# Performance work log

Hardware: AMD Instinct MI355X
Metric: run time of the kernel (lower is better)

The kernel has to match this reference:

```python
import jax, jax.numpy as jnp
import numpy as np

EPS = 1e-5  # InstanceNorm2d default eps (affine=False, biased var)

def setup_inputs() -> dict:
    key = jax.random.key(0)
    ks = jax.random.split(key, 16)
    B, N, KV, H = 16, 196, 960, 4
    chs = [64, 128, 256, 512]
    inp = {}
    inp['emb0'] = jax.random.normal(ks[0], (B, N, chs[0]), jnp.float32)
    inp['emb1'] = jax.random.normal(ks[1], (B, N, chs[1]), jnp.float32)
    inp['emb2'] = jax.random.normal(ks[2], (B, N, chs[2]), jnp.float32)
    inp['emb3'] = jax.random.normal(ks[3], (B, N, chs[3]), jnp.float32)
    inp['emb_all'] = jax.random.normal(ks[4], (B, N, KV), jnp.float32)
    for i, ch in enumerate(chs):
        inp[f'Wq{i}'] = jax.random.normal(ks[5 + i], (H, ch, ch), jnp.float32) * (1.0 / np.sqrt(ch))
        inp[f'Wo{i}'] = jax.random.normal(ks[9 + i], (ch, ch), jnp.float32) * (1.0 / np.sqrt(ch))
    inp['Wk'] = jax.random.normal(ks[13], (H, KV, KV), jnp.float32) * (1.0 / np.sqrt(KV))
    inp['Wv'] = jax.random.normal(ks[14], (H, KV, KV), jnp.float32) * (1.0 / np.sqrt(KV))
    return inp

def _attend(emb, Wq, Wo, K, V, inv_sqrt_kv):
    # Q: per-head Linear(ch,ch) then transpose(-1,-2) -> [B,H,ch,N]
    Q = jnp.einsum('bnc,hdc->bhdn', emb, Wq)
    # scores: [B,H,ch,KV]
    scores = jnp.einsum('bhdn,bhnj->bhdj', Q, K) * inv_sqrt_kv
    # InstanceNorm2d over the (ch, KV) plane per (batch, head), no affine
    m = scores.mean(axis=(-2, -1), keepdims=True)
    v = scores.var(axis=(-2, -1), keepdims=True)
    probs = jax.nn.softmax((scores - m) * jax.lax.rsqrt(v + EPS), axis=-1)
    # ctx = (probs @ V^T).permute(0,3,2,1).mean(dim=3) -> mean over heads: [B,N,ch]
    ctx = jnp.einsum('bhdj,bhnj->bnd', probs, V) / probs.shape[1]
    # out projection: nn.Linear(ch,ch) -> x @ Wo^T
    return jnp.einsum('bnd,ed->bne', ctx, Wo)

def reference(emb0, emb1, emb2, emb3, emb_all, Wq0, Wq1, Wq2, Wq3, Wk, Wv, Wo0, Wo1, Wo2, Wo3):
    KV = emb_all.shape[-1]
    inv_sqrt_kv = jnp.float32(1.0 / np.sqrt(KV))
    # multi-head K/V: stacked per-head Linear(KV,KV) -> [B,H,N,KV]
    K = jnp.einsum('bnk,hjk->bhnj', emb_all, Wk)
    V = jnp.einsum('bnk,hjk->bhnj', emb_all, Wv)
    o0 = _attend(emb0, Wq0, Wo0, K, V, inv_sqrt_kv)
    o1 = _attend(emb1, Wq1, Wo1, K, V, inv_sqrt_kv)
    o2 = _attend(emb2, Wq2, Wo2, K, V, inv_sqrt_kv)
    o3 = _attend(emb3, Wq3, Wo3, K, V, inv_sqrt_kv)
    return (o0, o1, o2, o3)
```

## Files before the change

kernel.cpp:

```cpp
#include <hip/hip_runtime.h>

typedef _Float16 half_t;
typedef _Float16 h8 __attribute__((ext_vector_type(8)));
typedef _Float16 h4 __attribute__((ext_vector_type(4)));
typedef float f4v __attribute__((ext_vector_type(4)));

__device__ __forceinline__ void async16(half_t* l, const half_t* g)
{
    __builtin_amdgcn_global_load_lds(
        (const __attribute__((address_space(1))) void*)g,
        (__attribute__((address_space(3))) void*)l,
        16, 0, 0);
}

struct PrepArgs {
    const float* src[15];
    half_t* dst[15];
    int n[15];
    int mode[15];
    int lg2[15];
};

__global__ __launch_bounds__(256) void prep_k(PrepArgs a)
{
    const int seg = blockIdx.y;
    const int i8 = (blockIdx.x * 256 + threadIdx.x) * 8;
    if (i8 >= a.n[seg]) return;
    const float* s = a.src[seg] + i8;
    f4v v0 = *(const f4v*)s;
    f4v v1 = *(const f4v*)(s + 4);
    h8 o;
    o[0] = (half_t)v0[0]; o[1] = (half_t)v0[1]; o[2] = (half_t)v0[2]; o[3] = (half_t)v0[3];
    o[4] = (half_t)v1[0]; o[5] = (half_t)v1[1]; o[6] = (half_t)v1[2]; o[7] = (half_t)v1[3];
    if (a.mode[seg] == 0) {
        *(h8*)(a.dst[seg] + i8) = o;
    } else {
        const int lg = a.lg2[seg], ch = 1 << lg;
        const int e = i8 >> lg, d = i8 & (ch - 1);
        half_t* base = a.dst[seg] + ((long long)e << (lg + 2)) + d;
        #pragma unroll
        for (int r = 0; r < 4; ++r) *(h8*)(base + r * ch) = o;
    }
}

__device__ __forceinline__ h8 ldtile(const half_t* __restrict__ base, int row, int kb,
                                     int ld, int rowLim, int Klim)
{
    h8 v = {0, 0, 0, 0, 0, 0, 0, 0};
    if (row >= rowLim) return v;
    const half_t* p = base + (long long)row * ld + kb;
    if (kb + 8 <= Klim) return *(const h8*)p;
    #pragma unroll
    for (int e = 0; e < 8; ++e) if (kb + e < Klim) v[e] = p[e];
    return v;
}

struct BP {
    const half_t* A[6]; const half_t* B[6]; void* C[6];
    int Mlim[6], Nlim[6], Klim[6], nKt[6], lda[6], ldb[6], ldc[6];
    int divA[6]; long long sAhi[6], sAlo[6];
    int divB[6]; long long sBhi[6], sBlo[6];
    int divC[6]; long long sChi[6], sClo[6];
    int outMode[6];
    float alpha[6];
    int mT[6], nT[6];
    int cumEnd[5];
    int totW;
};

__global__ __launch_bounds__(128)
void gemm_b(BP P)
{
    __shared__ __align__(16) half_t SM[64 * 72];
    half_t (*As)[32] = (half_t(*)[32])SM;
    half_t (*Bs)[32] = (half_t(*)[32])(SM + 2048);

    int b = blockIdx.x;
    int s = 0, basev = 0;
    #pragma unroll
    for (int i = 0; i < 5; ++i) if (b >= P.cumEnd[i]) { s = i + 1; basev = P.cumEnd[i]; }
    b -= basev;
    const int mTl = P.mT[s], nTl = P.nT[s];
    const int mt = b % mTl;
    const int t2 = b / mTl;
    const int nt = t2 % nTl;
    const int z  = t2 / nTl;

    const half_t* A  = P.A[s] + (long long)(z / P.divA[s]) * P.sAhi[s] + (long long)(z % P.divA[s]) * P.sAlo[s];
    const half_t* Bp = P.B[s] + (long long)(z / P.divB[s]) * P.sBhi[s] + (long long)(z % P.divB[s]) * P.sBlo[s];
    const int Mlim = P.Mlim[s], Klim = P.Klim[s], nKt = P.nKt[s];
    const int lda = P.lda[s], ldb = P.ldb[s], ldc = P.ldc[s];
    const float alpha = P.alpha[s];
    const int m0 = mt * 64, n0 = nt * 64;
    const int tid = threadIdx.x;
    const int lane = tid & 63, w = tid >> 6;
    const int l15 = lane & 15, q = lane >> 4;

    const int r0 = tid >> 2, kg = tid & 3;
    const int r1 = r0 + 32;

    f4v acc[4][2];
    #pragma unroll
    for (int i = 0; i < 4; ++i)
        #pragma unroll
        for (int j = 0; j < 2; ++j) acc[i][j] = (f4v){0.f, 0.f, 0.f, 0.f};

    for (int kt = 0; kt < nKt; ++kt) {
        const int kb = kt * 32 + kg * 8;
        h8 a0 = ldtile(A, m0 + r0, kb, lda, Mlim, Klim);
        h8 a1 = ldtile(A, m0 + r1, kb, lda, Mlim, Klim);
        h8 b0 = ldtile(Bp, n0 + r0, kb, ldb, 1 << 30, Klim);
        h8 b1 = ldtile(Bp, n0 + r1, kb, ldb, 1 << 30, Klim);
        __syncthreads();
        *(h8*)&As[r0][kg * 8] = a0;
        *(h8*)&As[r1][kg * 8] = a1;
        *(h8*)&Bs[r0][kg * 8] = b0;
        *(h8*)&Bs[r1][kg * 8] = b1;
        __syncthreads();
        h8 af[4], bf[2];
        #pragma unroll
        for (int mti = 0; mti < 4; ++mti) af[mti] = *(h8*)&As[mti * 16 + l15][q * 8];
        #pragma unroll
        for (int nti = 0; nti < 2; ++nti) bf[nti] = *(h8*)&Bs[w * 32 + nti * 16 + l15][q * 8];
        #pragma unroll
        for (int mti = 0; mti < 4; ++mti)
            #pragma unroll
            for (int nti = 0; nti < 2; ++nti)
                acc[mti][nti] = __builtin_amdgcn_mfma_f32_16x16x32_f16(af[mti], bf[nti], acc[mti][nti], 0, 0, 0);
    }

    float* Cz = (float*)P.C[s] + (long long)(z / P.divC[s]) * P.sChi[s] + (long long)(z % P.divC[s]) * P.sClo[s];
    #pragma unroll
    for (int mti = 0; mti < 4; ++mti)
        #pragma unroll
        for (int r = 0; r < 4; ++r) {
            const int row = m0 + mti * 16 + q * 4 + r;
            if (row < Mlim) {
                #pragma unroll
                for (int nti = 0; nti < 2; ++nti) {
                    const int col = n0 + w * 32 + nti * 16 + l15;
                    Cz[(long long)row * ldc + col] = acc[mti][nti][r] * alpha;
                }
            }
        }
}

__global__ __launch_bounds__(256, 3)
void gemm_w(BP P)
{
    __shared__ __align__(16) half_t SMEM[16384];

    const int per = gridDim.x >> 3;
    int wk = (blockIdx.x & 7) * per + (blockIdx.x >> 3);
    if (wk >= P.totW) return;
    int s = 0, basev = 0;
    #pragma unroll
    for (int i = 0; i < 5; ++i) if (wk >= P.cumEnd[i]) { s = i + 1; basev = P.cumEnd[i]; }
    wk -= basev;
    const int mTl = P.mT[s], nTl = P.nT[s];
    const int mt = wk % mTl;
    const int t2 = wk / mTl;
    const int nt = t2 % nTl;
    const int z  = t2 / nTl;

    const half_t* A  = P.A[s] + (long long)(z / P.divA[s]) * P.sAhi[s] + (long long)(z % P.divA[s]) * P.sAlo[s];
    const half_t* Bp = P.B[s] + (long long)(z / P.divB[s]) * P.sBhi[s] + (long long)(z % P.divB[s]) * P.sBlo[s];
    const int Mlim = P.Mlim[s], Nlim = P.Nlim[s], nKt = P.nKt[s];
    const int lda = P.lda[s], ldb = P.ldb[s], ldc = P.ldc[s];
    const float alpha = P.alpha[s];
    const int m0 = mt * 128, n0 = nt * 128;
    const int tid = threadIdx.x;
    const int lane = tid & 63, wv = tid >> 6;
    const int wm = wv & 1, wn = wv >> 1;
    const int l15 = lane & 15, q = lane >> 4;
    const int r0 = tid >> 2, kg = tid & 3;

    const int rA0 = min(m0 + r0,       Mlim - 1);
    const int rA1 = min(m0 + r0 + 64,  Mlim - 1);
    const int rB0 = min(n0 + r0,       Nlim - 1);
    const int rB1 = min(n0 + r0 + 64,  Nlim - 1);
    const half_t* gA0 = A  + (long long)rA0 * lda + kg * 8;
    const half_t* gA1 = A  + (long long)rA1 * lda + kg * 8;
    const half_t* gB0 = Bp + (long long)rB0 * ldb + kg * 8;
    const half_t* gB1 = Bp + (long long)rB1 * ldb + kg * 8;

    const int wb = wv * 512;

    f4v acc[4][4];
    #pragma unroll
    for (int i = 0; i < 4; ++i)
        #pragma unroll
        for (int j = 0; j < 4; ++j) acc[i][j] = (f4v){0.f, 0.f, 0.f, 0.f};

    auto stage = [&](int buf) {
        half_t* base = SMEM + buf * 8192;
        async16(base        + wb, gA0);
        async16(base + 2048 + wb, gA1);
        async16(base + 4096 + wb, gB0);
        async16(base + 6144 + wb, gB1);
        gA0 += 32; gA1 += 32; gB0 += 32; gB1 += 32;
    };
    auto compute = [&](int buf) {
        const half_t* As = SMEM + buf * 8192;
        const half_t* Bs = As + 4096;
        h8 af[4], bf[4];
        #pragma unroll
        for (int mi = 0; mi < 4; ++mi) af[mi] = *(const h8*)(As + (wm * 64 + mi * 16 + l15) * 32 + q * 8);
        #pragma unroll
        for (int ni = 0; ni < 4; ++ni) bf[ni] = *(const h8*)(Bs + (wn * 64 + ni * 16 + l15) * 32 + q * 8);
        #pragma unroll
        for (int mi = 0; mi < 4; ++mi)
            #pragma unroll
            for (int ni = 0; ni < 4; ++ni)
                acc[mi][ni] = __builtin_amdgcn_mfma_f32_16x16x32_f16(af[mi], bf[ni], acc[mi][ni], 0, 0, 0);
    };

    stage(0);
    __syncthreads();
    for (int kt = 0; kt < nKt; kt += 2) {
        stage(1);
        compute(0);
        __syncthreads();
        if (kt + 2 < nKt) stage(0);
        compute(1);
        __syncthreads();
    }

    if (P.outMode[s] == 1) {
        half_t* Cz = (half_t*)P.C[s] + (long long)(z / P.divC[s]) * P.sChi[s] + (long long)(z % P.divC[s]) * P.sClo[s];
        #pragma unroll
        for (int mi = 0; mi < 4; ++mi)
            #pragma unroll
            for (int r = 0; r < 4; ++r) {
                const int row = m0 + wm * 64 + mi * 16 + q * 4 + r;
                if (row < Mlim) {
                    #pragma unroll
                    for (int ni = 0; ni < 4; ++ni) {
                        const int col = n0 + wn * 64 + ni * 16 + l15;
                        if (col < Nlim) Cz[(long long)row * ldc + col] = (half_t)(acc[mi][ni][r] * alpha);
                    }
                }
            }
    } else {
        half_t (*T2)[128] = (half_t(*)[128])SMEM;
        half_t* Cz = (half_t*)P.C[s] + (long long)(z / P.divC[s]) * P.sChi[s] + (long long)(z % P.divC[s]) * P.sClo[s];
        #pragma unroll
        for (int mi = 0; mi < 4; ++mi)
            #pragma unroll
            for (int ni = 0; ni < 4; ++ni) {
                h4 pk;
                #pragma unroll
                for (int r = 0; r < 4; ++r) pk[r] = (half_t)(acc[mi][ni][r] * alpha);
                const int col = wn * 64 + ni * 16 + l15;
                const int g   = wm * 16 + mi * 4 + q;
                *(h4*)&T2[col][4 * (g ^ (col & 31))] = pk;
            }
        __syncthreads();
        {
            const int col  = tid >> 1;
            const int coff = (tid & 1) * 64;
            const int gb   = (tid & 1) * 16;
            const int mbase = m0 + coff;
            const int nfull = max(0, min(64, ldc - mbase)) >> 3;
            if (n0 + col < Nlim && nfull > 0) {
                half_t* rp = Cz + (long long)(n0 + col) * ldc + mbase;
                for (int j = 0; j < nfull; ++j) {
                    h4 lo = *(h4*)&T2[col][4 * ((gb + 2 * j)     ^ (col & 31))];
                    h4 hi = *(h4*)&T2[col][4 * ((gb + 2 * j + 1) ^ (col & 31))];
                    h8 v = {lo[0], lo[1], lo[2], lo[3], hi[0], hi[1], hi[2], hi[3]};
                    *(h8*)(rp + j * 8) = v;
                }
            }
        }
    }
}

struct ScP {
    const half_t* Qt[4];
    const half_t* KT;
    half_t* C[4];
    float* Part[4];
    int Mlim[4];
    long long sA[4], sC[4];
    float alpha;
};

__global__ __launch_bounds__(256)
void gemm_s(ScP P)
{
    __shared__ __align__(16) half_t As[128][232];
    __shared__ __align__(16) half_t Bs[128][72];
    __shared__ float red[8];

    const int per = gridDim.x >> 3;
    int wk = (blockIdx.x & 7) * per + (blockIdx.x >> 3);
    const int z = wk >> 3, r = wk & 7;
    int s, mt;
    if (r < 1)      { s = 0; mt = 0; }
    else if (r < 2) { s = 1; mt = 0; }
    else if (r < 4) { s = 2; mt = r - 2; }
    else            { s = 3; mt = r - 4; }
    const int b = z >> 2, h = z & 3;

    const half_t* A = P.Qt[s] + (long long)z * P.sA[s] + (long long)mt * 128 * 208;
    const half_t* B = P.KT + (long long)h * 3072000 + (long long)b * 196;
    const int rowLim = P.Mlim[s] - mt * 128;
    const float alpha = P.alpha;

    const int tid = threadIdx.x;
    const int lane = tid & 63, wv = tid >> 6;
    const int wm = wv & 1, wn = wv >> 1;
    const int l15 = lane & 15, q = lane >> 4;
    const int r0 = tid >> 2, kg = tid & 3;

    #pragma unroll
    for (int c = 0; c < 7; ++c) {
        const int kb = c * 32 + kg * 8;
        h8 a0 = ldtile(A, r0, kb, 208, rowLim, 196);
        h8 a1 = ldtile(A, r0 + 64, kb, 208, rowLim, 196);
        *(h8*)&As[r0][kb] = a0;
        *(h8*)&As[r0 + 64][kb] = a1;
    }

    half_t* Cz = P.C[s] + (long long)z * P.sC[s] + (long long)mt * 128 * 960;
    float sv = 0.f, qq = 0.f;

    for (int nt = 0; nt < 8; ++nt) {
        f4v acc[4][4];
        #pragma unroll
        for (int i = 0; i < 4; ++i)
            #pragma unroll
            for (int j = 0; j < 4; ++j) acc[i][j] = (f4v){0.f, 0.f, 0.f, 0.f};

        const int j0 = nt * 128;
        #pragma unroll
        for (int c2 = 0; c2 < 4; ++c2) {
            h8 b00 = ldtile(B, j0 + r0,      c2 * 64 + kg * 8,      3200, 960, 196);
            h8 b01 = ldtile(B, j0 + r0,      c2 * 64 + 32 + kg * 8, 3200, 960, 196);
            h8 b10 = ldtile(B, j0 + r0 + 64, c2 * 64 + kg * 8,      3200, 960, 196);
            h8 b11 = ldtile(B, j0 + r0 + 64, c2 * 64 + 32 + kg * 8, 3200, 960, 196);
            __syncthreads();
            *(h8*)&Bs[r0][kg * 8] = b00;
            *(h8*)&Bs[r0][32 + kg * 8] = b01;
            *(h8*)&Bs[r0 + 64][kg * 8] = b10;
            *(h8*)&Bs[r0 + 64][32 + kg * 8] = b11;
            __syncthreads();
            const int nkk = (c2 < 3) ? 2 : 1;
            for (int kk = 0; kk < nkk; ++kk) {
                const int base = c2 * 64 + kk * 32;
                h8 af[4], bf[4];
                #pragma unroll
                for (int mi = 0; mi < 4; ++mi) af[mi] = *(h8*)&As[wm * 64 + mi * 16 + l15][base + q * 8];
                #pragma unroll
                for (int ni = 0; ni < 4; ++ni) bf[ni] = *(h8*)&Bs[wn * 64 + ni * 16 + l15][kk * 32 + q * 8];
                #pragma unroll
                for (int mi = 0; mi < 4; ++mi)
                    #pragma unroll
                    for (int ni = 0; ni < 4; ++ni)
                        acc[mi][ni] = __builtin_amdgcn_mfma_f32_16x16x32_f16(af[mi], bf[ni], acc[mi][ni], 0, 0, 0);
            }
        }
        #pragma unroll
        for (int mi = 0; mi < 4; ++mi)
            #pragma unroll
            for (int rr = 0; rr < 4; ++rr) {
                const int rowl = wm * 64 + mi * 16 + q * 4 + rr;
                #pragma unroll
                for (int ni = 0; ni < 4; ++ni) {
                    const int col = j0 + wn * 64 + ni * 16 + l15;
                    const float v = acc[mi][ni][rr] * alpha;
                    sv += v; qq += v * v;
                    if (rowl < rowLim && col < 960)
                        Cz[(long long)rowl * 960 + col] = (half_t)v;
                }
            }
    }

    #pragma unroll
    for (int o = 32; o > 0; o >>= 1) {
        sv += __shfl_down(sv, o, 64);
        qq += __shfl_down(qq, o, 64);
    }
    if (lane == 0) { red[wv] = sv; red[4 + wv] = qq; }
    __syncthreads();
    if (tid == 0) {
        float* PO = P.Part[s] + (long long)z * 240 + mt * 2;
        PO[0] = red[0] + red[1] + red[2] + red[3];
        PO[1] = red[4] + red[5] + red[6] + red[7];
    }
}

struct CtxP {
    const half_t* V;
    const half_t* S[4];
    half_t* C[4];
    const float* Part[4];
    int ch[4];
    int nPart[4];
    float pinv[4];
};

__global__ __launch_bounds__(256)
void ctx_k(CtxP P)
{
    __shared__ __align__(16) half_t As[128][40];
    __shared__ __align__(16) half_t Bs[128][40];
    __shared__ float denomP[128][4];
    __shared__ float denom[128];

    const int per = gridDim.x >> 3;
    int wk = (blockIdx.x & 7) * per + (blockIdx.x >> 3);
    const int z = wk >> 4;
    const int r = wk & 15;
    int s, mt, nt;
    if (r < 2)      { s = 0; mt = r;            nt = 0; }
    else if (r < 4) { s = 1; mt = r - 2;        nt = 0; }
    else if (r < 8) { s = 2; mt = (r - 4) >> 1; nt = (r - 4) & 1; }
    else            { s = 3; mt = (r - 8) >> 2; nt = (r - 8) & 3; }
    const int b = z >> 2, h = z & 3;
    const int chS = P.ch[s];

    const float* part = P.Part[s] + (long long)z * 240;
    float Ssum = 0.f, Qsum = 0.f;
    for (int i = 0; i < P.nPart[s]; ++i) { Ssum += part[i * 2]; Qsum += part[i * 2 + 1]; }
    const float mn = Ssum * P.pinv[s];
    const float rs = rsqrtf(fmaxf(Qsum * P.pinv[s] - mn * mn, 0.f) + 1e-5f);

    const half_t* Av  = P.V + (long long)h * 3010560 + (long long)b * 188160;
    const half_t* Bsc = P.S[s] + (long long)z * 960 * chS;
    const int m0 = mt * 128, n0 = nt * 128;

    const int tid = threadIdx.x;
    const int lane = tid & 63, wv = tid >> 6;
    const int wm = wv & 1, wn = wv >> 1;
    const int l15 = lane & 15, q = lane >> 4;
    const int r0 = tid >> 2, kg = tid & 3;
    const int d0 = n0 + r0, d1 = n0 + r0 + 64;
    const bool ok0 = d0 < chS, ok1 = d1 < chS;

    f4v acc[4][4];
    #pragma unroll
    for (int i = 0; i < 4; ++i)
        #pragma unroll
        for (int j = 0; j < 4; ++j) acc[i][j] = (f4v){0.f, 0.f, 0.f, 0.f};

    float ds0 = 0.f, ds1 = 0.f;

    h8 a0n = ldtile(Av, m0 + r0, kg * 8, 960, 196, 960);
    h8 a1n = ldtile(Av, m0 + r0 + 64, kg * 8, 960, 196, 960);
    h8 s0n = {0,0,0,0,0,0,0,0}, s1n = {0,0,0,0,0,0,0,0};
    if (ok0) s0n = *(const h8*)(Bsc + (long long)d0 * 960 + kg * 8);
    if (ok1) s1n = *(const h8*)(Bsc + (long long)d1 * 960 + kg * 8);

    for (int kt = 0; kt < 30; ++kt) {
        h8 e0 = {0,0,0,0,0,0,0,0}, e1 = {0,0,0,0,0,0,0,0};
        if (ok0) {
            #pragma unroll
            for (int e = 0; e < 8; ++e) { float ev = __expf((float)s0n[e] * rs); ds0 += ev; e0[e] = (half_t)ev; }
        }
        if (ok1) {
            #pragma unroll
            for (int e = 0; e < 8; ++e) { float ev = __expf((float)s1n[e] * rs); ds1 += ev; e1[e] = (half_t)ev; }
        }
        h8 a0c = a0n, a1c = a1n;
        __syncthreads();
        *(h8*)&As[r0][kg * 8] = a0c;
        *(h8*)&As[r0 + 64][kg * 8] = a1c;
        *(h8*)&Bs[r0][kg * 8] = e0;
        *(h8*)&Bs[r0 + 64][kg * 8] = e1;
        __syncthreads();
        if (kt < 29) {
            const int kb = (kt + 1) * 32 + kg * 8;
            a0n = ldtile(Av, m0 + r0, kb, 960, 196, 960);
            a1n = ldtile(Av, m0 + r0 + 64, kb, 960, 196, 960);
            if (ok0) s0n = *(const h8*)(Bsc + (long long)d0 * 960 + kb);
            if (ok1) s1n = *(const h8*)(Bsc + (long long)d1 * 960 + kb);
        }
        h8 af[4], bf[4];
        #pragma unroll
        for (int mi = 0; mi < 4; ++mi) af[mi] = *(h8*)&As[wm * 64 + mi * 16 + l15][q * 8];
        #pragma unroll
        for (int ni = 0; ni < 4; ++ni) bf[ni] = *(h8*)&Bs[wn * 64 + ni * 16 + l15][q * 8];
        #pragma unroll
        for (int mi = 0; mi < 4; ++mi)
            #pragma unroll
            for (int ni = 0; ni < 4; ++ni)
                acc[mi][ni] = __builtin_amdgcn_mfma_f32_16x16x32_f16(af[mi], bf[ni], acc[mi][ni], 0, 0, 0);
    }

    denomP[r0][kg] = ds0;
    denomP[r0 + 64][kg] = ds1;
    __syncthreads();
    if (tid < 128) denom[tid] = denomP[tid][0] + denomP[tid][1] + denomP[tid][2] + denomP[tid][3];
    __syncthreads();

    half_t* Cz = P.C[s] + (long long)b * 784 * chS + (long long)h * chS;
    const int ldc = 4 * chS;
    #pragma unroll
    for (int ni = 0; ni < 4; ++ni) {
        const int coll = wn * 64 + ni * 16 + l15;
        const int col = n0 + coll;
        if (col < chS) {
            const float sc = 0.25f / denom[coll];
            #pragma unroll
            for (int mi = 0; mi < 4; ++mi)
                #pragma unroll
                for (int rr = 0; rr < 4; ++rr) {
                    const int row = m0 + wm * 64 + mi * 16 + q * 4 + rr;
                    if (row < 196)
                        Cz[(long long)row * ldc + col] = (half_t)(acc[mi][ni][rr] * sc);
                }
        }
    }
}

extern "C" void kernel_launch(void* const* d_in, const int* in_sizes, int n_in,
                              void* d_out, int out_size, void* d_ws, size_t ws_size,
                              hipStream_t stream)
{
    const float* emb[4]  = {(const float*)d_in[0], (const float*)d_in[1],
                            (const float*)d_in[2], (const float*)d_in[3]};
    const float* emb_all = (const float*)d_in[4];
    const float* Wq[4]   = {(const float*)d_in[5], (const float*)d_in[7],
                            (const float*)d_in[9], (const float*)d_in[11]};
    const float* Wo[4]   = {(const float*)d_in[6], (const float*)d_in[8],
                            (const float*)d_in[10], (const float*)d_in[12]};
    const float* Wk = (const float*)d_in[13];
    const float* Wv = (const float*)d_in[14];
    float* out = (float*)d_out;

    half_t* hb = (half_t*)d_ws;
    half_t* EAh = hb;
    half_t* Eh  = EAh + 3010560;
    half_t* Wkh = Eh  + 3010560;
    half_t* Wvh = Wkh + 3686400;
    half_t* Wqh = Wvh + 3686400;
    half_t* Wo4 = Wqh + 1392640;
    half_t* KT  = Wo4 + 1392640;
    half_t* Vh  = KT  + 12779520;
    half_t* QtT = Vh  + 12042240;
    half_t* Ctx = QtT + 12779520;
    half_t* Sch = Ctx + 12042240;
    float*  Part = (float*)(Sch + 58982400);

    const int  chs[4]   = {64, 128, 256, 512};
    const int  lg2c[4]  = {6, 7, 8, 9};
    const long long offE[4]   = {0, 200704, 602112, 1404928};
    const long long offQ[4]   = {0, 16384, 81920, 344064};
    const long long offQt[4]  = {0, 851968, 2555904, 5963776};
    const long long offSc[4]  = {0, 3932160, 11796480, 27525120};
    const long long offCtx[4] = {0, 802816, 2408448, 5619712};
    const long long ooff[4]   = {0, 200704, 602112, 1404928};
    const float inv_sqrt_kv = 0.03227486121839514f;

    PrepArgs pa;
    pa.src[0] = emb_all; pa.dst[0] = EAh; pa.n[0] = 3010560; pa.mode[0] = 0; pa.lg2[0] = 0;
    for (int i = 0; i < 4; ++i) {
        pa.src[1 + i] = emb[i]; pa.dst[1 + i] = Eh + offE[i];
        pa.n[1 + i] = (int)(3136LL * chs[i]); pa.mode[1 + i] = 0; pa.lg2[1 + i] = 0;
    }
    pa.src[5] = Wk; pa.dst[5] = Wkh; pa.n[5] = 3686400; pa.mode[5] = 0; pa.lg2[5] = 0;
    pa.src[6] = Wv; pa.dst[6] = Wvh; pa.n[6] = 3686400; pa.mode[6] = 0; pa.lg2[6] = 0;
    for (int i = 0; i < 4; ++i) {
        pa.src[7 + i] = Wq[i]; pa.dst[7 + i] = Wqh + offQ[i];
        pa.n[7 + i] = 4 * chs[i] * chs[i]; pa.mode[7 + i] = 0; pa.lg2[7 + i] = 0;
        pa.src[11 + i] = Wo[i]; pa.dst[11 + i] = Wo4 + offQ[i];
        pa.n[11 + i] = chs[i] * chs[i]; pa.mode[11 + i] = 1; pa.lg2[11 + i] = lg2c[i];
    }
    prep_k<<<dim3(1800, 15), 256, 0, stream>>>(pa);

    {
        BP p{};
        p.A[0] = EAh; p.B[0] = Wkh; p.C[0] = KT;
        p.Mlim[0] = 3136; p.Nlim[0] = 960; p.Klim[0] = 960; p.nKt[0] = 30;
        p.lda[0] = 960; p.ldb[0] = 960; p.ldc[0] = 3200;
        p.divA[0] = 1; p.sAhi[0] = 0; p.sAlo[0] = 0;
        p.divB[0] = 1; p.sBhi[0] = 921600; p.sBlo[0] = 0;
        p.divC[0] = 1; p.sChi[0] = 3072000; p.sClo[0] = 0;
        p.outMode[0] = 2; p.alpha[0] = 1.0f;
        p.mT[0] = 25; p.nT[0] = 8;
        p.A[1] = EAh; p.B[1] = Wvh; p.C[1] = Vh;
        p.Mlim[1] = 3136; p.Nlim[1] = 960; p.Klim[1] = 960; p.nKt[1] = 30;
        p.lda[1] = 960; p.ldb[1] = 960; p.ldc[1] = 960;
        p.divA[1] = 1; p.sAhi[1] = 0; p.sAlo[1] = 0;
        p.divB[1] = 1; p.sBhi[1] = 921600; p.sBlo[1] = 0;
        p.divC[1] = 1; p.sChi[1] = 3010560; p.sClo[1] = 0;
        p.outMode[1] = 1; p.alpha[1] = 1.0f;
        p.mT[1] = 25; p.nT[1] = 8;
        for (int i = 0; i < 4; ++i) {
            const int sl = 2 + i, ch = chs[i];
            p.A[sl] = Eh + offE[i]; p.B[sl] = Wqh + offQ[i]; p.C[sl] = QtT + offQt[i];
            p.Mlim[sl] = 196; p.Nlim[sl] = ch; p.Klim[sl] = ch; p.nKt[sl] = ch / 32;
            p.lda[sl] = ch; p.ldb[sl] = ch; p.ldc[sl] = 208;
            p.divA[sl] = 4; p.sAhi[sl] = 196LL * ch; p.sAlo[sl] = 0;
            p.divB[sl] = 4; p.sBhi[sl] = 0; p.sBlo[sl] = (long long)ch * ch;
            p.divC[sl] = 1; p.sChi[sl] = 208LL * ch; p.sClo[sl] = 0;
            p.outMode[sl] = 2; p.alpha[sl] = 1.0f;
            p.mT[sl] = 2; p.nT[sl] = (ch + 127) / 128;
        }
        int cum = 0;
        const int blocks[6] = {800, 800, 128, 128, 256, 512};
        for (int sl = 0; sl < 6; ++sl) { cum += blocks[sl]; if (sl < 5) p.cumEnd[sl] = cum; }
        p.totW = cum;
        gemm_w<<<2624, 256, 0, stream>>>(p);
    }

    {
        ScP p{};
        for (int s = 0; s < 4; ++s) {
            p.Qt[s] = QtT + offQt[s];
            p.C[s] = Sch + offSc[s];
            p.Part[s] = Part + (long long)s * 64 * 240;
            p.Mlim[s] = chs[s];
            p.sA[s] = 208LL * chs[s];
            p.sC[s] = 960LL * chs[s];
        }
        p.KT = KT;
        p.alpha = inv_sqrt_kv;
        gemm_s<<<512, 256, 0, stream>>>(p);
    }

    {
        CtxP p{};
        p.V = Vh;
        const int nP[4] = {1, 1, 2, 4};
        for (int s = 0; s < 4; ++s) {
            p.S[s] = Sch + offSc[s];
            p.C[s] = Ctx + offCtx[s];
            p.Part[s] = Part + (long long)s * 64 * 240;
            p.ch[s] = chs[s];
            p.nPart[s] = nP[s];
            p.pinv[s] = 1.0f / (chs[s] * 960);
        }
        ctx_k<<<1024, 256, 0, stream>>>(p);
    }

    {
        BP p{};
        int cum = 0;
        for (int s = 0; s < 4; ++s) {
            const int ch = chs[s];
            p.A[s] = Ctx + offCtx[s]; p.B[s] = Wo4 + offQ[s]; p.C[s] = out + ooff[s];
            p.Mlim[s] = 196; p.Nlim[s] = ch; p.Klim[s] = 4 * ch; p.nKt[s] = ch / 8;
            p.lda[s] = 4 * ch; p.ldb[s] = 4 * ch; p.ldc[s] = ch;
            p.divA[s] = 1; p.sAhi[s] = 784LL * ch; p.sAlo[s] = 0;
            p.divB[s] = 1; p.sBhi[s] = 0; p.sBlo[s] = 0;
            p.divC[s] = 1; p.sChi[s] = 196LL * ch; p.sClo[s] = 0;
            p.outMode[s] = 0; p.alpha[s] = 1.0f;
            p.mT[s] = 4; p.nT[s] = ch / 64;
            cum += 4 * (ch / 64) * 16;
            if (s < 3) p.cumEnd[s] = cum;
        }
        p.cumEnd[3] = p.cumEnd[4] = cum;
        p.totW = cum;
        gemm_b<<<960, 128, 0, stream>>>(p);
    }
}
```

Before: 418.8 us.

## Triple-buffer gemm_w loads with vmcnt waits and remap gemm_s block ordering

The weight GEMM moves from a double-buffered loop with full __syncthreads to a three-stage LDS ring, two tiles in flight. It uses explicit s_waitcnt vmcnt(4) plus a raw s_barrier so the next tile's async loads stay outstanding while the current one computes. This raises LDS per block from 32KB to 48KB, which with launch_bounds(256,3) may reduce resident blocks per CU. Separately, gemm_s now decodes its block index head-major (h outer, b inner), so blocks scheduled together share the same per-head K slice, aiming for better cache reuse.

```diff
diff --git a/kernel.cpp b/kernel.cpp
--- a/kernel.cpp
+++ b/kernel.cpp
@@ -148,7 +148,7 @@
 __global__ __launch_bounds__(256, 3)
 void gemm_w(BP P)
 {
-    __shared__ __align__(16) half_t SMEM[16384];
+    __shared__ __align__(16) half_t SMEM[24576];
 
     const int per = gridDim.x >> 3;
     int wk = (blockIdx.x & 7) * per + (blockIdx.x >> 3);
@@ -192,16 +192,16 @@
         #pragma unroll
         for (int j = 0; j < 4; ++j) acc[i][j] = (f4v){0.f, 0.f, 0.f, 0.f};
 
-    auto stage = [&](int buf) {
-        half_t* base = SMEM + buf * 8192;
+    auto stage = [&](int off) {
+        half_t* base = SMEM + off;
         async16(base        + wb, gA0);
         async16(base + 2048 + wb, gA1);
         async16(base + 4096 + wb, gB0);
         async16(base + 6144 + wb, gB1);
         gA0 += 32; gA1 += 32; gB0 += 32; gB1 += 32;
     };
-    auto compute = [&](int buf) {
-        const half_t* As = SMEM + buf * 8192;
+    auto compute = [&](int off) {
+        const half_t* As = SMEM + off;
         const half_t* Bs = As + 4096;
         h8 af[4], bf[4];
         #pragma unroll
@@ -215,15 +215,20 @@
                 acc[mi][ni] = __builtin_amdgcn_mfma_f32_16x16x32_f16(af[mi], bf[ni], acc[mi][ni], 0, 0, 0);
     };
 
-    stage(0);
-    __syncthreads();
-    for (int kt = 0; kt < nKt; kt += 2) {
-        stage(1);
-        compute(0);
-        __syncthreads();
-        if (kt + 2 < nKt) stage(0);
-        compute(1);
-        __syncthreads();
+    int bA = 0, bB = 8192, bC = 16384;
+    stage(bA);
+    stage(bB);
+    asm volatile("s_waitcnt vmcnt(4)" ::: "memory");
+    __builtin_amdgcn_s_barrier();
+    asm volatile("" ::: "memory");
+    for (int kt = 0; kt < nKt; ++kt) {
+        if (kt + 2 < nKt) stage(bC);
+        compute(bA);
+        if (kt + 2 < nKt) asm volatile("s_waitcnt vmcnt(4) lgkmcnt(0)" ::: "memory");
+        else              asm volatile("s_waitcnt vmcnt(0) lgkmcnt(0)" ::: "memory");
+        __builtin_amdgcn_s_barrier();
+        asm volatile("" ::: "memory");
+        int t = bA; bA = bB; bB = bC; bC = t;
     }
 
     if (P.outMode[s] == 1) {
@@ -294,15 +299,16 @@
 
     const int per = gridDim.x >> 3;
     int wk = (blockIdx.x & 7) * per + (blockIdx.x >> 3);
-    const int z = wk >> 3, r = wk & 7;
+    const int zl = wk >> 3, r = wk & 7;
     int s, mt;
     if (r < 1)      { s = 0; mt = 0; }
     else if (r < 2) { s = 1; mt = 0; }
     else if (r < 4) { s = 2; mt = r - 2; }
     else            { s = 3; mt = r - 4; }
-    const int b = z >> 2, h = z & 3;
-
-    const half_t* A = P.Qt[s] + (long long)z * P.sA[s] + (long long)mt * 128 * 208;
+    const int h = zl >> 4, b = zl & 15;
+    const int zq = b * 4 + h;
+
+    const half_t* A = P.Qt[s] + (long long)zq * P.sA[s] + (long long)mt * 128 * 208;
     const half_t* B = P.KT + (long long)h * 3072000 + (long long)b * 196;
     const int rowLim = P.Mlim[s] - mt * 128;
     const float alpha = P.alpha;
@@ -322,7 +328,7 @@
         *(h8*)&As[r0 + 64][kb] = a1;
     }
 
-    half_t* Cz = P.C[s] + (long long)z * P.sC[s] + (long long)mt * 128 * 960;
+    half_t* Cz = P.C[s] + (long long)zq * P.sC[s] + (long long)mt * 128 * 960;
     float sv = 0.f, qq = 0.f;
 
     for (int nt = 0; nt < 8; ++nt) {
@@ -384,7 +390,7 @@
     if (lane == 0) { red[wv] = sv; red[4 + wv] = qq; }
     __syncthreads();
     if (tid == 0) {
-        float* PO = P.Part[s] + (long long)z * 240 + mt * 2;
+        float* PO = P.Part[s] + (long long)zq * 240 + mt * 2;
         PO[0] = red[0] + red[1] + red[2] + red[3];
         PO[1] = red[4] + red[5] + red[6] + red[7];
     }
```

After: 412.0 us. Within noise of the previous version (-1.6%).
